# Optimization experiments

Hardware: AMD Instinct MI355X
Metric: run time of the kernel (lower is better)

Reference implementation:

```python
import jax, jax.numpy as jnp
import numpy as np

N, H, W = 128, 400, 400          # instances, feature canvas
MS = 28                          # mask_size = pooler_resolution*2
CT, CS = 80, 53                  # thing / stuff classes
STRIDE = 4                       # common_stride
HG, WG = 1600, 1600              # image-resolution gt panoptic
IGNORE = 255
LOSS_W = 1.0


def setup_inputs() -> dict:
    key = jax.random.key(0)
    ks = jax.random.split(key, 8)
    mask_logits = jax.random.normal(ks[0], (N, CT, MS, MS), jnp.float32)
    stuff_logit = jax.random.normal(ks[1], (CS, H, W), jnp.float32)
    thing_logit = jax.random.normal(ks[2], (CT, H, W), jnp.float32)
    # valid boxes in image pixel coords (x0,y0,x2,y2), width/height >= 16 px
    x0 = jax.random.uniform(ks[3], (N,), minval=0.0, maxval=1200.0)
    y0 = jax.random.uniform(ks[4], (N,), minval=0.0, maxval=1200.0)
    wh = jax.random.uniform(ks[5], (N, 2), minval=16.0, maxval=400.0)
    x2 = jnp.minimum(x0 + wh[:, 0], WG - 1.0)
    y2 = jnp.minimum(y0 + wh[:, 1], HG - 1.0)
    bbox = jnp.stack([x0, y0, x2, y2], axis=1).astype(jnp.float32)
    cls_idx = jax.random.randint(ks[6], (N,), 0, CT, dtype=jnp.int32)
    gt_panoptic = jax.random.randint(ks[7], (HG, WG), 0, CS + N, dtype=jnp.int32)
    return {"mask_logits": mask_logits, "stuff_logit": stuff_logit,
            "thing_logit": thing_logit, "bbox": bbox, "cls_idx": cls_idx,
            "gt_panoptic": gt_panoptic}


def _axis_sample(lo, size, grid, src_size):
    """Bilinear sampling coords along one axis (align_corners=False).
    lo: [N] box start (feat px, int); size: [N] box extent; grid: [G].
    Returns (idx0, idx1, frac) each [N, G]."""
    dst = grid[None, :].astype(jnp.float32) - lo[:, None].astype(jnp.float32)
    src = (dst + 0.5) * (src_size / size[:, None].astype(jnp.float32)) - 0.5
    f = jnp.floor(src)
    t = src - f
    i0 = jnp.clip(f, 0, src_size - 1).astype(jnp.int32)
    i1 = jnp.clip(f + 1, 0, src_size - 1).astype(jnp.int32)
    return i0, i1, t


def reference(mask_logits, stuff_logit, thing_logit, bbox, cls_idx, gt_panoptic):
    # _separate_fetch_logits: gather per-instance class channel -> [N, MS, MS]
    ml = mask_logits[jnp.arange(N), cls_idx]

    # _unmap_mask_logit_single: boxes -> feat coords (.long() == floor, boxes >= 0)
    bl = jnp.floor(bbox / STRIDE).astype(jnp.int32)
    x0b, y0b, x2b, y2b = bl[:, 0], bl[:, 1], bl[:, 2], bl[:, 3]
    hh = y2b - y0b + 1
    ww = x2b - x0b + 1
    ys = jnp.arange(H, dtype=jnp.int32)
    xs = jnp.arange(W, dtype=jnp.int32)

    i0, i1, ty = _axis_sample(y0b, hh, ys, MS)   # [N, H]
    j0, j1, tx = _axis_sample(x0b, ww, xs, MS)   # [N, W]

    # separable bilinear: rows [N, H, MS] then cols [N, H, W]
    r0 = jnp.take_along_axis(ml, jnp.broadcast_to(i0[:, :, None], (N, H, MS)), axis=1)
    r1 = jnp.take_along_axis(ml, jnp.broadcast_to(i1[:, :, None], (N, H, MS)), axis=1)
    rows = r0 * (1.0 - ty)[:, :, None] + r1 * ty[:, :, None]
    c0 = jnp.take_along_axis(rows, jnp.broadcast_to(j0[:, None, :], (N, H, W)), axis=2)
    c1 = jnp.take_along_axis(rows, jnp.broadcast_to(j1[:, None, :], (N, H, W)), axis=2)
    val = c0 * (1.0 - tx)[:, None, :] + c1 * tx[:, None, :]

    vy = (ys[None, :] >= jnp.maximum(y0b, 0)[:, None]) & (ys[None, :] <= jnp.minimum(y2b, H - 1)[:, None])
    vx = (xs[None, :] >= jnp.maximum(x0b, 0)[:, None]) & (xs[None, :] <= jnp.minimum(x2b, W - 1)[:, None])
    thing_mask_logit = jnp.where(vy[:, :, None] & vx[:, None, :], val, 0.0)

    # _crop_thing_logit_single: int()/round() based crop window
    bf = bbox / STRIDE
    cx1 = bf[:, 0].astype(jnp.int32)
    cy1 = bf[:, 1].astype(jnp.int32)
    cx2 = (jnp.round(bf[:, 2]) + 1.0).astype(jnp.int32)
    cy2 = (jnp.round(bf[:, 3]) + 1.0).astype(jnp.int32)
    my = (ys[None, :] >= cy1[:, None]) & (ys[None, :] < cy2[:, None])
    mx = (xs[None, :] >= cx1[:, None]) & (xs[None, :] < cx2[:, None])
    thing_sem_logit = jnp.where(my[:, :, None] & mx[:, None, :], thing_logit[cls_idx], 0.0)

    pan_logit = jnp.concatenate(
        [stuff_logit[None], (thing_mask_logit + thing_sem_logit)[None]], axis=1)

    # gt nearest-downsample to feat_size, then CE with ignore_index
    iy = jnp.floor(jnp.arange(H) * (HG / H)).astype(jnp.int32)
    ix = jnp.floor(jnp.arange(W) * (WG / W)).astype(jnp.int32)
    gt_ds = gt_panoptic[iy[:, None], ix[None, :]][None]          # [1, H, W]
    logp = jax.nn.log_softmax(pan_logit, axis=1)
    tgt = jnp.clip(gt_ds, 0, CS + N - 1)
    nll = -jnp.take_along_axis(logp, tgt[:, None], axis=1)[:, 0]  # [1, H, W]
    valid = gt_ds != IGNORE
    pan_loss = LOSS_W * jnp.sum(jnp.where(valid, nll, 0.0)) / jnp.maximum(
        jnp.sum(valid).astype(jnp.float32), 1.0)
    return pan_logit, pan_loss
```

## Files before the change

### kernel.cpp

```cpp
#include <hip/hip_runtime.h>
#include <math.h>

#define N_   128
#define H_   400
#define W_   400
#define MS_  28
#define CT_  80
#define CS_  53
#define HW_  (H_*W_)
#define NCH_ (CS_ + N_)
#define WG_  1600
#define IGN_ 255
#define PPT_ 2
#define BT_  256
#define PPB_ (BT_*PPT_)
#define GX_  ((HW_ + PPB_ - 1)/PPB_)

typedef float f2 __attribute__((ext_vector_type(2)));

struct NParam {
  int vy_lo, vy_hi, vx_lo, vx_hi;
  int cy1, cy2, cx1, cx2;
  float sy, sx;
  int y0b, x0b;
  int mlbase, thbase;
  int pad0, pad1;
};

__device__ unsigned int g_done;
__device__ float        g_part[GX_*2];

#define AG_ST(p, v) __hip_atomic_store((p), (v), __ATOMIC_RELAXED, __HIP_MEMORY_SCOPE_AGENT)
#define AG_LD(p)    __hip_atomic_load((p), __ATOMIC_RELAXED, __HIP_MEMORY_SCOPE_AGENT)

__device__ __forceinline__ void lse_update(float v, float& m, float& s) {
  float d = v - m;
  float e = __expf(-fabsf(d));
  s = (d > 0.0f) ? fmaf(s, e, 1.0f) : (s + e);
  m = fmaxf(m, v);
}

__global__ __launch_bounds__(256) void main_kernel(
    const float* __restrict__ mask_logits,
    const float* __restrict__ stuff_logit,
    const float* __restrict__ thing_logit,
    const float* __restrict__ bbox,
    const int*   __restrict__ cls_idx,
    const int*   __restrict__ gt,
    float* __restrict__ out)
{
  __shared__ NParam spar[N_];
  __shared__ int4   sbox[N_];
  __shared__ float  red[8];
  __shared__ unsigned s_fin;
  int tid = threadIdx.x;
  if (tid < N_) {
    int n = tid;
    float b0 = bbox[4*n+0]*0.25f, b1 = bbox[4*n+1]*0.25f,
          b2 = bbox[4*n+2]*0.25f, b3 = bbox[4*n+3]*0.25f;
    int x0b = (int)floorf(b0), y0b = (int)floorf(b1);
    int x2b = (int)floorf(b2), y2b = (int)floorf(b3);
    int hh = y2b - y0b + 1, ww = x2b - x0b + 1;
    NParam p;
    p.vy_lo = max(y0b, 0); p.vy_hi = min(y2b, H_-1);
    p.vx_lo = max(x0b, 0); p.vx_hi = min(x2b, W_-1);
    p.cy1 = (int)b1; p.cx1 = (int)b0;
    p.cy2 = (int)(rintf(b3) + 1.0f);
    p.cx2 = (int)(rintf(b2) + 1.0f);
    p.sy = 28.0f / (float)hh; p.sx = 28.0f / (float)ww;
    p.y0b = y0b; p.x0b = x0b;
    int cls = cls_idx[n];
    p.mlbase = (n*CT_ + cls)*(MS_*MS_);
    p.thbase = cls*HW_;
    p.pad0 = 0; p.pad1 = 0;
    spar[n] = p;
    sbox[n] = make_int4(min(p.vy_lo, p.cy1), max(p.vy_hi, p.cy2 - 1),
                        min(p.vx_lo, p.cx1), max(p.vx_hi, p.cx2 - 1));
  }
  __syncthreads();

  int pix0 = (blockIdx.x*BT_ + tid)*PPT_;
  bool act = (pix0 < HW_);
  float nll = 0.0f, cnt = 0.0f;

  if (act) {
    int y  = pix0 / W_;
    int xb = pix0 - y*W_;

    int graw[PPT_], tcs[PPT_];
    #pragma unroll
    for (int k = 0; k < PPT_; ++k) {
      int g = gt[y*(4*WG_) + (xb + k)*4];
      graw[k] = g;
      tcs[k] = min(max(g, 0), NCH_-1);
    }

    float mv[PPT_], sv[PPT_], vts[PPT_];
    #pragma unroll
    for (int k = 0; k < PPT_; ++k) { mv[k] = -INFINITY; sv[k] = 0.0f; vts[k] = 0.0f; }
    int zc = 0;

    for (int c = 0; c < CS_; ++c) {
      f2 v = *(const f2*)(stuff_logit + c*HW_ + pix0);
      *(f2*)(out + c*HW_ + pix0) = v;
      #pragma unroll
      for (int k = 0; k < PPT_; ++k) {
        lse_update(v[k], mv[k], sv[k]);
        if (c == tcs[k]) vts[k] = v[k];
      }
    }
    for (int c = CS_; c < NCH_; ++c) {
      int n = c - CS_;
      int4 u = sbox[n];
      bool rej = (y < u.x) | (y > u.y) | (xb > u.w) | (xb + PPT_ - 1 < u.z);
      if (__all(rej)) {
        f2 z = {0.0f, 0.0f};
        *(f2*)(out + c*HW_ + pix0) = z;
        ++zc;
        continue;
      }
      NParam p = spar[n];
      float vv[PPT_] = {0.0f, 0.0f};
      if (y >= p.cy1 && y < p.cy2 && xb < p.cx2 && xb+PPT_-1 >= p.cx1) {
        f2 t = *(const f2*)(thing_logit + p.thbase + pix0);
        #pragma unroll
        for (int k = 0; k < PPT_; ++k) {
          int x = xb + k;
          if (x >= p.cx1 && x < p.cx2) vv[k] = t[k];
        }
      }
      if (y >= p.vy_lo && y <= p.vy_hi && xb <= p.vx_hi && xb+PPT_-1 >= p.vx_lo) {
        float srcy = ((float)(y - p.y0b) + 0.5f)*p.sy - 0.5f;
        float fy = floorf(srcy); float ty = srcy - fy;
        int i0 = (int)fminf(fmaxf(fy,        0.0f), (float)(MS_-1));
        int i1 = (int)fminf(fmaxf(fy + 1.0f, 0.0f), (float)(MS_-1));
        const float* r0p = mask_logits + p.mlbase + i0*MS_;
        const float* r1p = mask_logits + p.mlbase + i1*MS_;
        #pragma unroll
        for (int k = 0; k < PPT_; ++k) {
          int x = xb + k;
          if (x >= p.vx_lo && x <= p.vx_hi) {
            float srcx = ((float)(x - p.x0b) + 0.5f)*p.sx - 0.5f;
            float fx = floorf(srcx); float tx = srcx - fx;
            int j0 = (int)fminf(fmaxf(fx,        0.0f), (float)(MS_-1));
            int j1 = (int)fminf(fmaxf(fx + 1.0f, 0.0f), (float)(MS_-1));
            float r0 = r0p[j0]*(1.0f - tx) + r0p[j1]*tx;
            float r1 = r1p[j0]*(1.0f - tx) + r1p[j1]*tx;
            vv[k] += r0*(1.0f - ty) + r1*ty;
          }
        }
      }
      f2 ov = {vv[0], vv[1]};
      *(f2*)(out + c*HW_ + pix0) = ov;
      #pragma unroll
      for (int k = 0; k < PPT_; ++k) {
        lse_update(vv[k], mv[k], sv[k]);
        if (c == tcs[k]) vts[k] = vv[k];
      }
    }

    float zcf = (float)zc;
    #pragma unroll
    for (int k = 0; k < PPT_; ++k) {
      float m = mv[k], s = sv[k];
      if (zc > 0) {
        if (m >= 0.0f) { s = fmaf(zcf, __expf(-m), s); }
        else           { s = fmaf(s, __expf(m), zcf); m = 0.0f; }
      }
      bool valid = (graw[k] != IGN_);
      nll += valid ? (m + __logf(s) - vts[k]) : 0.0f;
      cnt += valid ? 1.0f : 0.0f;
    }
  }

  for (int off = 32; off >= 1; off >>= 1) {
    nll += __shfl_down(nll, off, 64);
    cnt += __shfl_down(cnt, off, 64);
  }
  int lane = tid & 63, wid = tid >> 6;
  if (lane == 0) { red[wid*2] = nll; red[wid*2+1] = cnt; }
  __syncthreads();
  if (tid == 0) {
    float ts  = red[0] + red[2] + red[4] + red[6];
    float tcn = red[1] + red[3] + red[5] + red[7];
    AG_ST(&g_part[blockIdx.x*2],     ts);
    AG_ST(&g_part[blockIdx.x*2 + 1], tcn);
    asm volatile("s_waitcnt vmcnt(0)" ::: "memory");
    unsigned d = __hip_atomic_fetch_add(&g_done, 1u,
                                        __ATOMIC_RELAXED, __HIP_MEMORY_SCOPE_AGENT);
    s_fin = ((d % (unsigned)GX_) == (unsigned)(GX_-1)) ? 1u : 0u;
  }
  __syncthreads();
  if (s_fin) {
    float a = 0.0f, b = 0.0f;
    if (tid < GX_)        { a += AG_LD(&g_part[tid*2]);        b += AG_LD(&g_part[tid*2 + 1]); }
    if (tid + BT_ < GX_)  { a += AG_LD(&g_part[(tid+BT_)*2]);  b += AG_LD(&g_part[(tid+BT_)*2 + 1]); }
    for (int off = 32; off >= 1; off >>= 1) {
      a += __shfl_down(a, off, 64);
      b += __shfl_down(b, off, 64);
    }
    if (lane == 0) { red[wid*2] = a; red[wid*2+1] = b; }
    __syncthreads();
    if (tid == 0) {
      float ts  = red[0] + red[2] + red[4] + red[6];
      float tcn = red[1] + red[3] + red[5] + red[7];
      out[NCH_*HW_] = ts / fmaxf(tcn, 1.0f);
    }
  }
}

extern "C" void kernel_launch(void* const* d_in, const int* in_sizes, int n_in,
                              void* d_out, int out_size, void* d_ws, size_t ws_size,
                              hipStream_t stream) {
  const float* mask_logits = (const float*)d_in[0];
  const float* stuff_logit = (const float*)d_in[1];
  const float* thing_logit = (const float*)d_in[2];
  const float* bbox        = (const float*)d_in[3];
  const int*   cls_idx     = (const int*)d_in[4];
  const int*   gt          = (const int*)d_in[5];
  float* out = (float*)d_out;

  main_kernel<<<GX_, BT_, 0, stream>>>(mask_logits, stuff_logit, thing_logit,
                                       bbox, cls_idx, gt, out);
}
```

Baseline: 237.1 us.

## Split channel loop across eight wave groups per pixel tile with LDS logsumexp merge

Each block now covers 128 pixels with 8 waves. Each wave handles a strided subset of the channels (stuff channels c = grp, grp+8, ...; thing channels assigned round-robin), and the per-wave partial logsumexp results are merged through LDS. The goal is more memory-level parallelism and more waves in flight per pixel than one thread walking all 181 channels serially. It also prefetches the next stuff channel and switches to nontemporal loads and stores for the streamed logits and output. In exchange it adds an LDS reduction, an extra barrier, and a second gt read, and it leaves 128 threads of reduction work per block.

```diff
diff --git a/kernel.cpp b/kernel.cpp
--- a/kernel.cpp
+++ b/kernel.cpp
@@ -11,12 +11,17 @@
 #define NCH_ (CS_ + N_)
 #define WG_  1600
 #define IGN_ 255
+#define G_   8
+#define NTH_G 16
 #define PPT_ 2
-#define BT_  256
-#define PPB_ (BT_*PPT_)
-#define GX_  ((HW_ + PPB_ - 1)/PPB_)
+#define BT_  512
+#define TPX_ 128
+#define GX_  (HW_/TPX_)
 
 typedef float f2 __attribute__((ext_vector_type(2)));
+
+#define NT_LD(p)    __builtin_nontemporal_load(p)
+#define NT_ST(v, p) __builtin_nontemporal_store((v), (p))
 
 struct NParam {
   int vy_lo, vy_hi, vx_lo, vx_hi;
@@ -40,7 +45,7 @@
   m = fmaxf(m, v);
 }
 
-__global__ __launch_bounds__(256) void main_kernel(
+__global__ __launch_bounds__(512) void main_kernel(
     const float* __restrict__ mask_logits,
     const float* __restrict__ stuff_logit,
     const float* __restrict__ thing_logit,
@@ -51,7 +56,9 @@
 {
   __shared__ NParam spar[N_];
   __shared__ int4   sbox[N_];
-  __shared__ float  red[8];
+  __shared__ float  lp_lds[G_][TPX_];
+  __shared__ float  vt_lds[TPX_];
+  __shared__ float  red[16];
   __shared__ unsigned s_fin;
   int tid = threadIdx.x;
   if (tid < N_) {
@@ -79,86 +86,106 @@
   }
   __syncthreads();
 
-  int pix0 = (blockIdx.x*BT_ + tid)*PPT_;
-  bool act = (pix0 < HW_);
-  float nll = 0.0f, cnt = 0.0f;
-
-  if (act) {
-    int y  = pix0 / W_;
-    int xb = pix0 - y*W_;
-
-    int graw[PPT_], tcs[PPT_];
+  int grp  = tid >> 6;
+  int lane = tid & 63;
+  int pix0 = blockIdx.x*TPX_ + lane*PPT_;
+  int y  = pix0 / W_;
+  int xb = pix0 - y*W_;
+  int cth_start = CS_ + ((grp - (CS_ & 7)) & 7);
+
+  int tcs[PPT_];
+  #pragma unroll
+  for (int k = 0; k < PPT_; ++k) {
+    int g = gt[y*(4*WG_) + (xb + k)*4];
+    tcs[k] = min(max(g, 0), NCH_-1);
+  }
+
+  float mv[PPT_], sv[PPT_], vts[PPT_];
+  #pragma unroll
+  for (int k = 0; k < PPT_; ++k) { mv[k] = -INFINITY; sv[k] = 0.0f; vts[k] = 0.0f; }
+
+  {
+    int c = grp;
+    if (c < CS_) {
+      f2 v = NT_LD((const f2*)(stuff_logit + c*HW_ + pix0));
+      for (;;) {
+        int cn = c + G_;
+        bool more = (cn < CS_);
+        f2 vn;
+        if (more) vn = NT_LD((const f2*)(stuff_logit + cn*HW_ + pix0));
+        NT_ST(v, (f2*)(out + c*HW_ + pix0));
+        #pragma unroll
+        for (int k = 0; k < PPT_; ++k) {
+          lse_update(v[k], mv[k], sv[k]);
+          if (c == tcs[k]) vts[k] = v[k];
+        }
+        if (!more) break;
+        v = vn; c = cn;
+      }
+    }
+  }
+
+  unsigned amask = 0u;
+  #pragma unroll
+  for (int i = 0; i < NTH_G; ++i) {
+    int4 u = sbox[cth_start - CS_ + 8*i];
+    bool rej = (y < u.x) | (y > u.y) | (xb > u.w) | (xb + PPT_ - 1 < u.z);
+    if (!__all(rej)) amask |= (1u << i);
+  }
+  amask = __builtin_amdgcn_readfirstlane(amask);
+  int zc = NTH_G - __popc(amask);
+  {
+    f2 z = {0.0f, 0.0f};
+    for (int i = 0; i < NTH_G; ++i) {
+      if (!((amask >> i) & 1u))
+        NT_ST(z, (f2*)(out + (cth_start + 8*i)*HW_ + pix0));
+    }
+  }
+  unsigned am = amask;
+  while (am) {
+    int i = __builtin_ctz(am); am &= am - 1u;
+    int cc = cth_start + 8*i;
+    NParam p = spar[cc - CS_];
+    float vv[PPT_] = {0.0f, 0.0f};
+    if (y >= p.cy1 && y < p.cy2 && xb < p.cx2 && xb+PPT_-1 >= p.cx1) {
+      f2 t = NT_LD((const f2*)(thing_logit + p.thbase + pix0));
+      #pragma unroll
+      for (int k = 0; k < PPT_; ++k) {
+        int x = xb + k;
+        if (x >= p.cx1 && x < p.cx2) vv[k] = t[k];
+      }
+    }
+    if (y >= p.vy_lo && y <= p.vy_hi && xb <= p.vx_hi && xb+PPT_-1 >= p.vx_lo) {
+      float srcy = ((float)(y - p.y0b) + 0.5f)*p.sy - 0.5f;
+      float fy = floorf(srcy); float ty = srcy - fy;
+      int i0 = (int)fminf(fmaxf(fy,        0.0f), (float)(MS_-1));
+      int i1 = (int)fminf(fmaxf(fy + 1.0f, 0.0f), (float)(MS_-1));
+      const float* r0p = mask_logits + p.mlbase + i0*MS_;
+      const float* r1p = mask_logits + p.mlbase + i1*MS_;
+      #pragma unroll
+      for (int k = 0; k < PPT_; ++k) {
+        int x = xb + k;
+        if (x >= p.vx_lo && x <= p.vx_hi) {
+          float srcx = ((float)(x - p.x0b) + 0.5f)*p.sx - 0.5f;
+          float fx = floorf(srcx); float tx = srcx - fx;
+          int j0 = (int)fminf(fmaxf(fx,        0.0f), (float)(MS_-1));
+          int j1 = (int)fminf(fmaxf(fx + 1.0f, 0.0f), (float)(MS_-1));
+          float r0 = r0p[j0]*(1.0f - tx) + r0p[j1]*tx;
+          float r1 = r1p[j0]*(1.0f - tx) + r1p[j1]*tx;
+          vv[k] += r0*(1.0f - ty) + r1*ty;
+        }
+      }
+    }
+    f2 ov = {vv[0], vv[1]};
+    NT_ST(ov, (f2*)(out + cc*HW_ + pix0));
     #pragma unroll
     for (int k = 0; k < PPT_; ++k) {
-      int g = gt[y*(4*WG_) + (xb + k)*4];
-      graw[k] = g;
-      tcs[k] = min(max(g, 0), NCH_-1);
-    }
-
-    float mv[PPT_], sv[PPT_], vts[PPT_];
-    #pragma unroll
-    for (int k = 0; k < PPT_; ++k) { mv[k] = -INFINITY; sv[k] = 0.0f; vts[k] = 0.0f; }
-    int zc = 0;
-
-    for (int c = 0; c < CS_; ++c) {
-      f2 v = *(const f2*)(stuff_logit + c*HW_ + pix0);
-      *(f2*)(out + c*HW_ + pix0) = v;
-      #pragma unroll
-      for (int k = 0; k < PPT_; ++k) {
-        lse_update(v[k], mv[k], sv[k]);
-        if (c == tcs[k]) vts[k] = v[k];
-      }
-    }
-    for (int c = CS_; c < NCH_; ++c) {
-      int n = c - CS_;
-      int4 u = sbox[n];
-      bool rej = (y < u.x) | (y > u.y) | (xb > u.w) | (xb + PPT_ - 1 < u.z);
-      if (__all(rej)) {
-        f2 z = {0.0f, 0.0f};
-        *(f2*)(out + c*HW_ + pix0) = z;
-        ++zc;
-        continue;
-      }
-      NParam p = spar[n];
-      float vv[PPT_] = {0.0f, 0.0f};
-      if (y >= p.cy1 && y < p.cy2 && xb < p.cx2 && xb+PPT_-1 >= p.cx1) {
-        f2 t = *(const f2*)(thing_logit + p.thbase + pix0);
-        #pragma unroll
-        for (int k = 0; k < PPT_; ++k) {
-          int x = xb + k;
-          if (x >= p.cx1 && x < p.cx2) vv[k] = t[k];
-        }
-      }
-      if (y >= p.vy_lo && y <= p.vy_hi && xb <= p.vx_hi && xb+PPT_-1 >= p.vx_lo) {
-        float srcy = ((float)(y - p.y0b) + 0.5f)*p.sy - 0.5f;
-        float fy = floorf(srcy); float ty = srcy - fy;
-        int i0 = (int)fminf(fmaxf(fy,        0.0f), (float)(MS_-1));
-        int i1 = (int)fminf(fmaxf(fy + 1.0f, 0.0f), (float)(MS_-1));
-        const float* r0p = mask_logits + p.mlbase + i0*MS_;
-        const float* r1p = mask_logits + p.mlbase + i1*MS_;
-        #pragma unroll
-        for (int k = 0; k < PPT_; ++k) {
-          int x = xb + k;
-          if (x >= p.vx_lo && x <= p.vx_hi) {
-            float srcx = ((float)(x - p.x0b) + 0.5f)*p.sx - 0.5f;
-            float fx = floorf(srcx); float tx = srcx - fx;
-            int j0 = (int)fminf(fmaxf(fx,        0.0f), (float)(MS_-1));
-            int j1 = (int)fminf(fmaxf(fx + 1.0f, 0.0f), (float)(MS_-1));
-            float r0 = r0p[j0]*(1.0f - tx) + r0p[j1]*tx;
-            float r1 = r1p[j0]*(1.0f - tx) + r1p[j1]*tx;
-            vv[k] += r0*(1.0f - ty) + r1*ty;
-          }
-        }
-      }
-      f2 ov = {vv[0], vv[1]};
-      *(f2*)(out + c*HW_ + pix0) = ov;
-      #pragma unroll
-      for (int k = 0; k < PPT_; ++k) {
-        lse_update(vv[k], mv[k], sv[k]);
-        if (c == tcs[k]) vts[k] = vv[k];
-      }
-    }
-
+      lse_update(vv[k], mv[k], sv[k]);
+      if (cc == tcs[k]) vts[k] = vv[k];
+    }
+  }
+
+  {
     float zcf = (float)zc;
     #pragma unroll
     for (int k = 0; k < PPT_; ++k) {
@@ -167,22 +194,41 @@
         if (m >= 0.0f) { s = fmaf(zcf, __expf(-m), s); }
         else           { s = fmaf(s, __expf(m), zcf); m = 0.0f; }
       }
-      bool valid = (graw[k] != IGN_);
-      nll += valid ? (m + __logf(s) - vts[k]) : 0.0f;
-      cnt += valid ? 1.0f : 0.0f;
-    }
+      lp_lds[grp][lane*PPT_ + k] = m + __logf(s);
+      if ((tcs[k] & (G_-1)) == grp) vt_lds[lane*PPT_ + k] = vts[k];
+    }
+  }
+  __syncthreads();
+
+  float nll = 0.0f, cnt = 0.0f;
+  if (tid < TPX_) {
+    int p = blockIdx.x*TPX_ + tid;
+    float m = lp_lds[0][tid], s = 1.0f;
+    #pragma unroll
+    for (int g = 1; g < G_; ++g) {
+      float lg = lp_lds[g][tid];
+      float d = lg - m;
+      float e = __expf(-fabsf(d));
+      s = (d > 0.0f) ? fmaf(s, e, 1.0f) : (s + e);
+      m = fmaxf(m, lg);
+    }
+    int yy = p / W_;
+    int xx = p - yy*W_;
+    int gv = gt[yy*(4*WG_) + xx*4];
+    bool valid = (gv != IGN_);
+    nll = valid ? (m + __logf(s) - vt_lds[tid]) : 0.0f;
+    cnt = valid ? 1.0f : 0.0f;
   }
 
   for (int off = 32; off >= 1; off >>= 1) {
     nll += __shfl_down(nll, off, 64);
     cnt += __shfl_down(cnt, off, 64);
   }
-  int lane = tid & 63, wid = tid >> 6;
-  if (lane == 0) { red[wid*2] = nll; red[wid*2+1] = cnt; }
+  int wid = tid >> 6;
+  if ((tid & 63) == 0) { red[wid*2] = nll; red[wid*2+1] = cnt; }
   __syncthreads();
   if (tid == 0) {
-    float ts  = red[0] + red[2] + red[4] + red[6];
-    float tcn = red[1] + red[3] + red[5] + red[7];
+    float ts = red[0] + red[2], tcn = red[1] + red[3];
     AG_ST(&g_part[blockIdx.x*2],     ts);
     AG_ST(&g_part[blockIdx.x*2 + 1], tcn);
     asm volatile("s_waitcnt vmcnt(0)" ::: "memory");
@@ -193,17 +239,20 @@
   __syncthreads();
   if (s_fin) {
     float a = 0.0f, b = 0.0f;
-    if (tid < GX_)        { a += AG_LD(&g_part[tid*2]);        b += AG_LD(&g_part[tid*2 + 1]); }
-    if (tid + BT_ < GX_)  { a += AG_LD(&g_part[(tid+BT_)*2]);  b += AG_LD(&g_part[(tid+BT_)*2 + 1]); }
+    for (int i = tid; i < GX_; i += BT_) {
+      a += AG_LD(&g_part[i*2]);
+      b += AG_LD(&g_part[i*2 + 1]);
+    }
     for (int off = 32; off >= 1; off >>= 1) {
       a += __shfl_down(a, off, 64);
       b += __shfl_down(b, off, 64);
     }
-    if (lane == 0) { red[wid*2] = a; red[wid*2+1] = b; }
+    if ((tid & 63) == 0) { red[wid*2] = a; red[wid*2+1] = b; }
     __syncthreads();
     if (tid == 0) {
-      float ts  = red[0] + red[2] + red[4] + red[6];
-      float tcn = red[1] + red[3] + red[5] + red[7];
+      float ts = 0.0f, tcn = 0.0f;
+      #pragma unroll
+      for (int i = 0; i < 8; ++i) { ts += red[i*2]; tcn += red[i*2+1]; }
       out[NCH_*HW_] = ts / fmaxf(tcn, 1.0f);
     }
   }
```

Result: faster. 214.0 us (-9.8%).
